# Kernel optimization log

Hardware: AMD Instinct MI355X
Metric: run time of the kernel (lower is better)

The kernel has to match this reference:

```python
import jax, jax.numpy as jnp
import numpy as np

DX = 1.0  # voxel_spacing

def _grad(t, axis):
    """Central difference along `axis` with replicate (Neumann) boundaries.
    Matches F.pad(mode='replicate') + conv3d with a +/-0.5 stencil."""
    pad = [(0, 0)] * t.ndim
    pad[axis] = (1, 1)
    p = jnp.pad(t, pad, mode='edge')
    n = p.shape[axis]
    fwd = jax.lax.slice_in_dim(p, 2, n, axis=axis)
    bwd = jax.lax.slice_in_dim(p, 0, n - 2, axis=axis)
    return (fwd - bwd) * (0.5 / DX)

# axis mapping for [B, C, D, H, W]: grad_x -> W (4), grad_y -> H (3), grad_z -> D (2)
_AXES = (4, 3, 2)

def setup_inputs() -> dict:
    key = jax.random.key(0)
    k1, k2, k3 = jax.random.split(key, 3)
    shape = (4, 1, 192, 192, 192)
    u = jax.random.uniform(k1, shape, dtype=jnp.float32)
    D = jax.random.uniform(k2, shape, dtype=jnp.float32)
    rho = jax.random.uniform(k3, shape, dtype=jnp.float32)
    return {"u": u, "D": D, "rho": rho}

def reference(u, D, rho):
    # div(D * grad(u))
    div = jnp.zeros_like(u)
    for ax in _AXES:
        flux = D * _grad(u, ax)
        div = div + _grad(flux, ax)
    # du/dt = div(D grad u) + rho * u * (1 - u)
    return div + rho * u * (1.0 - u)
```

## Files before the change

### kernel.cpp

```cpp
#include <hip/hip_runtime.h>


#define NX 192

__global__ __launch_bounds__(192)
void fk_kernel(const float* __restrict__ u,
               const float* __restrict__ Dd,
               const float* __restrict__ rho,
               float* __restrict__ out)
{
    const int x = threadIdx.x;
    int row = blockIdx.x;
    const int y = row % NX;
    row /= NX;
    const int z = row % NX;
    const int b = row / NX;

    const int base = ((b * NX + z) * NX + y) * NX + x;

    const float uc = u[base];

    auto divterm = [&](int c, int stride) -> float {
        const int n = NX;
        const int jp  = (c + 1 < n) ? (c + 1) : (n - 1);
        const int jm  = (c - 1 > 0) ? (c - 1) : 0;
        const int jpp = (jp + 1 < n) ? (jp + 1) : (n - 1);
        const int jpm = jp - 1;
        const int jmp = jm + 1;
        const int jmm = (jm - 1 > 0) ? (jm - 1) : 0;

        const float fp = Dd[base + (jp - c) * stride] *
                         (u[base + (jpp - c) * stride] - u[base + (jpm - c) * stride]);
        const float fm = Dd[base + (jm - c) * stride] *
                         (u[base + (jmp - c) * stride] - u[base + (jmm - c) * stride]);
        return (fp - fm) * 0.25f;
    };

    const float dx = divterm(x, 1);
    const float dy = divterm(y, NX);
    const float dz = divterm(z, NX * NX);

    const float reaction = rho[base] * uc * (1.0f - uc);

    out[base] = dx + dy + dz + reaction;
}

extern "C" void kernel_launch(void* const* d_in, const int* in_sizes, int n_in,
                              void* d_out, int out_size, void* d_ws, size_t ws_size,
                              hipStream_t stream) {
    const float* u   = (const float*)d_in[0];
    const float* Dd  = (const float*)d_in[1];
    const float* rho = (const float*)d_in[2];
    float* out = (float*)d_out;

    const int B = 4;
    const int rows = B * NX * NX;

    fk_kernel<<<rows, NX, 0, stream>>>(u, Dd, rho, out);
}
```

Measured before the change: 125.8 us.

## Vectorize stencil with float4 per thread and 4-row blocks

Each thread now computes four consecutive x outputs using float4 loads for u, D, rho and the y/z neighbor rows, with a fast interior path for the x stencil that reuses loaded values. Blocks become 48x4 threads covering four y rows, so neighboring rows share cache lines. This cuts the number of load instructions and redundant per-element neighbor loads in a memory-bound stencil. Boundary threads use a scalar fallback path, and fewer total threads may reduce latency hiding.

```diff
diff --git a/kernel.cpp b/kernel.cpp
--- a/kernel.cpp
+++ b/kernel.cpp
@@ -9,40 +9,98 @@
                const float* __restrict__ rho,
                float* __restrict__ out)
 {
-    const int x = threadIdx.x;
-    int row = blockIdx.x;
-    const int y = row % NX;
-    row /= NX;
-    const int z = row % NX;
-    const int b = row / NX;
+    const int tx = threadIdx.x;
+    const int ty = threadIdx.y;
+    int bid = blockIdx.x;
+    const int ytile = bid % 48;  bid /= 48;
+    const int z = bid % NX;
+    const int b = bid / NX;
+    const int y = ytile * 4 + ty;
+    const int x0 = tx * 4;
 
-    const int base = ((b * NX + z) * NX + y) * NX + x;
+    const int rowb = ((b * NX + z) * NX + y) * NX;
+    const int base = rowb + x0;
 
-    const float uc = u[base];
+    const float4 uc = *(const float4*)(u   + base);
+    const float4 dc = *(const float4*)(Dd  + base);
+    const float4 rc = *(const float4*)(rho + base);
 
-    auto divterm = [&](int c, int stride) -> float {
-        const int n = NX;
-        const int jp  = (c + 1 < n) ? (c + 1) : (n - 1);
-        const int jm  = (c - 1 > 0) ? (c - 1) : 0;
-        const int jpp = (jp + 1 < n) ? (jp + 1) : (n - 1);
+    float divx[4];
+    if (tx > 0 && tx < 47) {
+        const float um2 = u[base - 2], um1 = u[base - 1];
+        const float up1 = u[base + 4], up2 = u[base + 5];
+        const float dm1 = Dd[base - 1], dp1 = Dd[base + 4];
+        const float w[8] = {um2, um1, uc.x, uc.y, uc.z, uc.w, up1, up2};
+        const float d6[6] = {dm1, dc.x, dc.y, dc.z, dc.w, dp1};
+        #pragma unroll
+        for (int i = 0; i < 4; ++i) {
+            const float fp = d6[i + 2] * (w[i + 4] - w[i + 2]);
+            const float fm = d6[i]     * (w[i + 2] - w[i]);
+            divx[i] = (fp - fm) * 0.25f;
+        }
+    } else {
+        #pragma unroll
+        for (int i = 0; i < 4; ++i) {
+            const int c   = x0 + i;
+            const int jp  = (c + 1 < NX) ? (c + 1) : (NX - 1);
+            const int jm  = (c - 1 > 0) ? (c - 1) : 0;
+            const int jpp = (jp + 1 < NX) ? (jp + 1) : (NX - 1);
+            const int jpm = jp - 1;
+            const int jmp = jm + 1;
+            const int jmm = (jm - 1 > 0) ? (jm - 1) : 0;
+            const float fp = Dd[rowb + jp] * (u[rowb + jpp] - u[rowb + jpm]);
+            const float fm = Dd[rowb + jm] * (u[rowb + jmp] - u[rowb + jmm]);
+            divx[i] = (fp - fm) * 0.25f;
+        }
+    }
+
+    float4 divy4;
+    {
+        const int jp  = (y + 1 < NX) ? (y + 1) : (NX - 1);
+        const int jm  = (y - 1 > 0) ? (y - 1) : 0;
+        const int jpp = (jp + 1 < NX) ? (jp + 1) : (NX - 1);
         const int jpm = jp - 1;
         const int jmp = jm + 1;
         const int jmm = (jm - 1 > 0) ? (jm - 1) : 0;
+        const float4 upp = *(const float4*)(u  + base + (jpp - y) * NX);
+        const float4 upm = *(const float4*)(u  + base + (jpm - y) * NX);
+        const float4 ump = *(const float4*)(u  + base + (jmp - y) * NX);
+        const float4 umm = *(const float4*)(u  + base + (jmm - y) * NX);
+        const float4 djp = *(const float4*)(Dd + base + (jp  - y) * NX);
+        const float4 djm = *(const float4*)(Dd + base + (jm  - y) * NX);
+        divy4.x = (djp.x * (upp.x - upm.x) - djm.x * (ump.x - umm.x)) * 0.25f;
+        divy4.y = (djp.y * (upp.y - upm.y) - djm.y * (ump.y - umm.y)) * 0.25f;
+        divy4.z = (djp.z * (upp.z - upm.z) - djm.z * (ump.z - umm.z)) * 0.25f;
+        divy4.w = (djp.w * (upp.w - upm.w) - djm.w * (ump.w - umm.w)) * 0.25f;
+    }
 
-        const float fp = Dd[base + (jp - c) * stride] *
-                         (u[base + (jpp - c) * stride] - u[base + (jpm - c) * stride]);
-        const float fm = Dd[base + (jm - c) * stride] *
-                         (u[base + (jmp - c) * stride] - u[base + (jmm - c) * stride]);
-        return (fp - fm) * 0.25f;
-    };
+    float4 divz4;
+    {
+        const int S   = NX * NX;
+        const int jp  = (z + 1 < NX) ? (z + 1) : (NX - 1);
+        const int jm  = (z - 1 > 0) ? (z - 1) : 0;
+        const int jpp = (jp + 1 < NX) ? (jp + 1) : (NX - 1);
+        const int jpm = jp - 1;
+        const int jmp = jm + 1;
+        const int jmm = (jm - 1 > 0) ? (jm - 1) : 0;
+        const float4 upp = *(const float4*)(u  + base + (jpp - z) * S);
+        const float4 upm = *(const float4*)(u  + base + (jpm - z) * S);
+        const float4 ump = *(const float4*)(u  + base + (jmp - z) * S);
+        const float4 umm = *(const float4*)(u  + base + (jmm - z) * S);
+        const float4 djp = *(const float4*)(Dd + base + (jp  - z) * S);
+        const float4 djm = *(const float4*)(Dd + base + (jm  - z) * S);
+        divz4.x = (djp.x * (upp.x - upm.x) - djm.x * (ump.x - umm.x)) * 0.25f;
+        divz4.y = (djp.y * (upp.y - upm.y) - djm.y * (ump.y - umm.y)) * 0.25f;
+        divz4.z = (djp.z * (upp.z - upm.z) - djm.z * (ump.z - umm.z)) * 0.25f;
+        divz4.w = (djp.w * (upp.w - upm.w) - djm.w * (ump.w - umm.w)) * 0.25f;
+    }
 
-    const float dx = divterm(x, 1);
-    const float dy = divterm(y, NX);
-    const float dz = divterm(z, NX * NX);
-
-    const float reaction = rho[base] * uc * (1.0f - uc);
-
-    out[base] = dx + dy + dz + reaction;
+    float4 o;
+    o.x = divx[0] + divy4.x + divz4.x + rc.x * uc.x * (1.0f - uc.x);
+    o.y = divx[1] + divy4.y + divz4.y + rc.y * uc.y * (1.0f - uc.y);
+    o.z = divx[2] + divy4.z + divz4.z + rc.z * uc.z * (1.0f - uc.z);
+    o.w = divx[3] + divy4.w + divz4.w + rc.w * uc.w * (1.0f - uc.w);
+    *(float4*)(out + base) = o;
 }
 
 extern "C" void kernel_launch(void* const* d_in, const int* in_sizes, int n_in,
@@ -54,7 +112,7 @@
     float* out = (float*)d_out;
 
     const int B = 4;
-    const int rows = B * NX * NX;
-
-    fk_kernel<<<rows, NX, 0, stream>>>(u, Dd, rho, out);
+    dim3 block(48, 4, 1);
+    const int grid = B * NX * (NX / 4);
+    fk_kernel<<<grid, block, 0, stream>>>(u, Dd, rho, out);
 }
```

Result: slower. 143.7 us (+14.2%).

## Stream along z with register sliding window and float4 vectorized stencil

Applied to the files above, without the earlier changes.

Each thread now handles four x-points and marches through a chunk of 16 z-planes. The z-neighbours of u and D are kept in a rotating set of registers, so each plane is read once for the z-direction stencil instead of repeatedly. Loads and the output store use float4 vectors, and the x-halo comes from short neighbouring loads. The aim is to cut redundant global and cache traffic in this memory-bound stencil, at the cost of more registers, per-chunk z-halo reloads and extra boundary-handling branches.

```diff
diff --git a/kernel.cpp b/kernel.cpp
--- a/kernel.cpp
+++ b/kernel.cpp
@@ -1,48 +1,132 @@
 #include <hip/hip_runtime.h>
 
 
-#define NX 192
+#define NX  192
+#define SP  (NX * NX)
+#define ZCH 16
 
-__global__ __launch_bounds__(192)
+__global__ __launch_bounds__(192, 4)
 void fk_kernel(const float* __restrict__ u,
                const float* __restrict__ Dd,
                const float* __restrict__ rho,
                float* __restrict__ out)
 {
-    const int x = threadIdx.x;
-    int row = blockIdx.x;
-    const int y = row % NX;
-    row /= NX;
-    const int z = row % NX;
-    const int b = row / NX;
+    const int tx = threadIdx.x;
+    const int ty = threadIdx.y;
+    int bid = blockIdx.x;
+    const int ytile = bid % (NX / 4);   bid /= (NX / 4);
+    const int zc    = bid % (NX / ZCH); bid /= (NX / ZCH);
+    const int b     = bid;
+    const int y  = ytile * 4 + ty;
+    const int x0 = tx * 4;
+    const int z0 = zc * ZCH;
 
-    const int base = ((b * NX + z) * NX + y) * NX + x;
+    const int jpY  = (y + 1 < NX) ? y + 1 : NX - 1;
+    const int jmY  = (y - 1 > 0) ? y - 1 : 0;
+    const int jppY = (jpY + 1 < NX) ? jpY + 1 : NX - 1;
+    const int jpmY = jpY - 1;
+    const int jmpY = jmY + 1;
+    const int jmmY = (jmY - 1 > 0) ? jmY - 1 : 0;
+    const bool ld_jpm = (jpmY != y);
+    const bool ld_jmp = (jmpY != y);
+    const int o_jpp = (jppY - y) * NX;
+    const int o_jmm = (jmmY - y) * NX;
+    const int o_jpm = (jpmY - y) * NX;
+    const int o_jmp = (jmpY - y) * NX;
+    const int o_jp  = (jpY  - y) * NX;
+    const int o_jm  = (jmY  - y) * NX;
 
-    const float uc = u[base];
+    const int col0 = ((b * NX + z0) * NX + y) * NX + x0;
+    const float* pu = u   + col0;
+    const float* pd = Dd  + col0;
+    const float* pr = rho + col0;
+    float*       po = out + col0;
 
-    auto divterm = [&](int c, int stride) -> float {
-        const int n = NX;
-        const int jp  = (c + 1 < n) ? (c + 1) : (n - 1);
-        const int jm  = (c - 1 > 0) ? (c - 1) : 0;
-        const int jpp = (jp + 1 < n) ? (jp + 1) : (n - 1);
-        const int jpm = jp - 1;
-        const int jmp = jm + 1;
-        const int jmm = (jm - 1 > 0) ? (jm - 1) : 0;
+    const int zm1 = (z0 - 1 > 0) ? z0 - 1 : 0;
+    const int zm2 = (z0 - 2 > 0) ? z0 - 2 : 0;
+    float4 uz0 = *(const float4*)(pu + (zm2 - z0) * SP);
+    float4 uz1 = *(const float4*)(pu + (zm1 - z0) * SP);
+    float4 uz2 = *(const float4*)(pu);
+    float4 uz3 = *(const float4*)(pu + SP);
+    float4 uz4 = *(const float4*)(pu + 2 * SP);
+    float4 dz0 = *(const float4*)(pd + (zm1 - z0) * SP);
+    float4 dz1 = *(const float4*)(pd);
+    float4 dz2 = *(const float4*)(pd + SP);
 
-        const float fp = Dd[base + (jp - c) * stride] *
-                         (u[base + (jpp - c) * stride] - u[base + (jpm - c) * stride]);
-        const float fm = Dd[base + (jm - c) * stride] *
-                         (u[base + (jmp - c) * stride] - u[base + (jmm - c) * stride]);
-        return (fp - fm) * 0.25f;
-    };
+    #pragma unroll 4
+    for (int z = z0; z < z0 + ZCH; ++z) {
+        const int zp3 = (z + 3 < NX) ? z + 3 : NX - 1;
+        const int zp2 = (z + 2 < NX) ? z + 2 : NX - 1;
+        const float4 unx = *(const float4*)(pu + (zp3 - z) * SP);
+        const float4 dnx = *(const float4*)(pd + (zp2 - z) * SP);
+        const float4 rc  = *(const float4*)(pr);
 
-    const float dx = divterm(x, 1);
-    const float dy = divterm(y, NX);
-    const float dz = divterm(z, NX * NX);
+        const float4 u_jpp = *(const float4*)(pu + o_jpp);
+        const float4 u_jmm = *(const float4*)(pu + o_jmm);
+        const float4 d_jp  = *(const float4*)(pd + o_jp);
+        const float4 d_jm  = *(const float4*)(pd + o_jm);
+        float4 u_jpm = uz2, u_jmp = uz2;
+        if (ld_jpm) u_jpm = *(const float4*)(pu + o_jpm);
+        if (ld_jmp) u_jmp = *(const float4*)(pu + o_jmp);
 
-    const float reaction = rho[base] * uc * (1.0f - uc);
+        float um2, um1, up1, up2, dm1, dp1;
+        if (tx > 0) {
+            const float2 t = *(const float2*)(pu - 2);
+            um2 = t.x; um1 = t.y; dm1 = pd[-1];
+        } else { um2 = uz2.x; um1 = uz2.x; dm1 = dz1.x; }
+        if (tx < NX / 4 - 1) {
+            const float2 t = *(const float2*)(pu + 4);
+            up1 = t.x; up2 = t.y; dp1 = pd[4];
+        } else { up1 = uz2.w; up2 = uz2.w; dp1 = dz1.w; }
 
-    out[base] = dx + dy + dz + reaction;
+        const float w[8]  = {um2, um1, uz2.x, uz2.y, uz2.z, uz2.w, up1, up2};
+        const float d6[6] = {dm1, dz1.x, dz1.y, dz1.z, dz1.w, dp1};
+        float divx[4];
+        #pragma unroll
+        for (int i = 0; i < 4; ++i) {
+            const float fp = d6[i + 2] * (w[i + 4] - w[i + 2]);
+            const float fm = d6[i]     * (w[i + 2] - w[i]);
+            divx[i] = (fp - fm) * 0.25f;
+        }
+        if (tx == 0)
+            divx[0] = (d6[2] * (w[4] - w[2]) - dz1.x * (uz2.y - uz2.x)) * 0.25f;
+        if (tx == NX / 4 - 1)
+            divx[3] = (dz1.w * (uz2.w - uz2.z) - d6[3] * (w[5] - w[3])) * 0.25f;
+
+        float4 divy;
+        divy.x = (d_jp.x * (u_jpp.x - u_jpm.x) - d_jm.x * (u_jmp.x - u_jmm.x)) * 0.25f;
+        divy.y = (d_jp.y * (u_jpp.y - u_jpm.y) - d_jm.y * (u_jmp.y - u_jmm.y)) * 0.25f;
+        divy.z = (d_jp.z * (u_jpp.z - u_jpm.z) - d_jm.z * (u_jmp.z - u_jmm.z)) * 0.25f;
+        divy.w = (d_jp.w * (u_jpp.w - u_jpm.w) - d_jm.w * (u_jmp.w - u_jmm.w)) * 0.25f;
+
+        const bool zlo = (z == 0), zhi = (z == NX - 1);
+        float4 divz;
+        {
+            const float apx = zhi ? uz2.x : uz4.x, bpx = zhi ? uz1.x : uz2.x;
+            const float apy = zhi ? uz2.y : uz4.y, bpy = zhi ? uz1.y : uz2.y;
+            const float apz = zhi ? uz2.z : uz4.z, bpz = zhi ? uz1.z : uz2.z;
+            const float apw = zhi ? uz2.w : uz4.w, bpw = zhi ? uz1.w : uz2.w;
+            const float amx = zlo ? uz3.x : uz2.x, bmx = zlo ? uz2.x : uz0.x;
+            const float amy = zlo ? uz3.y : uz2.y, bmy = zlo ? uz2.y : uz0.y;
+            const float amz = zlo ? uz3.z : uz2.z, bmz = zlo ? uz2.z : uz0.z;
+            const float amw = zlo ? uz3.w : uz2.w, bmw = zlo ? uz2.w : uz0.w;
+            divz.x = (dz2.x * (apx - bpx) - dz0.x * (amx - bmx)) * 0.25f;
+            divz.y = (dz2.y * (apy - bpy) - dz0.y * (amy - bmy)) * 0.25f;
+            divz.z = (dz2.z * (apz - bpz) - dz0.z * (amz - bmz)) * 0.25f;
+            divz.w = (dz2.w * (apw - bpw) - dz0.w * (amw - bmw)) * 0.25f;
+        }
+
+        float4 o;
+        o.x = divx[0] + divy.x + divz.x + rc.x * uz2.x * (1.0f - uz2.x);
+        o.y = divx[1] + divy.y + divz.y + rc.y * uz2.y * (1.0f - uz2.y);
+        o.z = divx[2] + divy.z + divz.z + rc.z * uz2.z * (1.0f - uz2.z);
+        o.w = divx[3] + divy.w + divz.w + rc.w * uz2.w * (1.0f - uz2.w);
+        *(float4*)po = o;
+
+        uz0 = uz1; uz1 = uz2; uz2 = uz3; uz3 = uz4; uz4 = unx;
+        dz0 = dz1; dz1 = dz2; dz2 = dnx;
+        pu += SP; pd += SP; pr += SP; po += SP;
+    }
 }
 
 extern "C" void kernel_launch(void* const* d_in, const int* in_sizes, int n_in,
@@ -54,7 +138,7 @@
     float* out = (float*)d_out;
 
     const int B = 4;
-    const int rows = B * NX * NX;
-
-    fk_kernel<<<rows, NX, 0, stream>>>(u, Dd, rho, out);
+    dim3 block(NX / 4, 4, 1);
+    const int grid = B * (NX / ZCH) * (NX / 4);
+    fk_kernel<<<grid, block, 0, stream>>>(u, Dd, rho, out);
 }
```

Measured after the change: 134.5 us. 6.9% more time.

## Tile 3D stencil in shared memory with z-marching rolling slab buffers

Applied to the files above, without the earlier changes.

Replaces the one-thread-per-voxel kernel, which made many redundant global loads per output, with 64x16 xy tiles that march through 24-slice z chunks. A rolling five-slab u buffer and three-slab D buffer live in LDS, the next slice is prefetched into registers, and each thread computes two x-adjacent outputs with float2 LDS and global access. Global traffic drops to roughly one read per input element plus halos. The costs are large LDS use per block, which limits occupancy, two barriers per z step, and a grid of only 1152 blocks.

```diff
diff --git a/kernel.cpp b/kernel.cpp
--- a/kernel.cpp
+++ b/kernel.cpp
@@ -1,48 +1,168 @@
 #include <hip/hip_runtime.h>
 
 
-#define NX 192
+#define NX   192
+#define SP   (NX * NX)
+#define TX   64
+#define TY   16
+#define ZC   24
+#define LROW 68
+#define SLAB (20 * LROW)
 
-__global__ __launch_bounds__(192)
+#define LD2(p, o) (*(const float2*)((p) + (o)))
+
+__global__ __launch_bounds__(512, 4)
 void fk_kernel(const float* __restrict__ u,
                const float* __restrict__ Dd,
                const float* __restrict__ rho,
                float* __restrict__ out)
 {
-    const int x = threadIdx.x;
-    int row = blockIdx.x;
-    const int y = row % NX;
-    row /= NX;
-    const int z = row % NX;
-    const int b = row / NX;
+    __shared__ float Ush[5 * SLAB];
+    __shared__ float Dsh[3 * SLAB];
 
-    const int base = ((b * NX + z) * NX + y) * NX + x;
+    const int tx  = threadIdx.x;
+    const int ty  = threadIdx.y;
+    const int tid = ty * 32 + tx;
 
-    const float uc = u[base];
+    int bid = blockIdx.x;
+    const int xt = bid % 3;  bid /= 3;
+    const int yt = bid % 12; bid /= 12;
+    const int zc = bid % 8;  bid /= 8;
+    const int b  = bid;
 
-    auto divterm = [&](int c, int stride) -> float {
-        const int n = NX;
-        const int jp  = (c + 1 < n) ? (c + 1) : (n - 1);
-        const int jm  = (c - 1 > 0) ? (c - 1) : 0;
-        const int jpp = (jp + 1 < n) ? (jp + 1) : (n - 1);
-        const int jpm = jp - 1;
-        const int jmp = jm + 1;
-        const int jmm = (jm - 1 > 0) ? (jm - 1) : 0;
+    const int x0 = xt * TX, y0 = yt * TY, z0 = zc * ZC;
 
-        const float fp = Dd[base + (jp - c) * stride] *
-                         (u[base + (jpp - c) * stride] - u[base + (jpm - c) * stride]);
-        const float fm = Dd[base + (jm - c) * stride] *
-                         (u[base + (jmp - c) * stride] - u[base + (jmm - c) * stride]);
-        return (fp - fm) * 0.25f;
-    };
+    const size_t vol = (size_t)b * NX * SP;
+    const float* ub = u   + vol;
+    const float* db = Dd  + vol;
+    const float* rb = rho + vol;
+    float*       ob = out + vol;
 
-    const float dx = divterm(x, 1);
-    const float dy = divterm(y, NX);
-    const float dz = divterm(z, NX * NX);
+    int g0, g1, g2;
+    {
+        #pragma unroll
+        for (int k = 0; k < 3; ++k) {
+            const int p = tid + 512 * k;
+            const int pp = (p < SLAB) ? p : 0;
+            const int r = pp / LROW, c = pp % LROW;
+            int gy = y0 + r - 2; gy = gy < 0 ? 0 : (gy > NX - 1 ? NX - 1 : gy);
+            int gx = x0 + c - 2; gx = gx < 0 ? 0 : (gx > NX - 1 ? NX - 1 : gx);
+            const int go = gy * NX + gx;
+            if (k == 0) g0 = go; else if (k == 1) g1 = go; else g2 = go;
+        }
+    }
+    const bool a2 = (tid < SLAB - 1024);
 
-    const float reaction = rho[base] * uc * (1.0f - uc);
+    #pragma unroll
+    for (int s = 0; s < 5; ++s) {
+        int pz = z0 - 2 + s; pz = pz < 0 ? 0 : pz;
+        const float* src = ub + (size_t)pz * SP;
+        Ush[s * SLAB + tid]       = src[g0];
+        Ush[s * SLAB + tid + 512] = src[g1];
+        if (a2) Ush[s * SLAB + tid + 1024] = src[g2];
+    }
+    #pragma unroll
+    for (int s = 0; s < 3; ++s) {
+        int pz = z0 - 1 + s; pz = pz < 0 ? 0 : pz;
+        const float* src = db + (size_t)pz * SP;
+        Dsh[s * SLAB + tid]       = src[g0];
+        Dsh[s * SLAB + tid + 512] = src[g1];
+        if (a2) Dsh[s * SLAB + tid + 1024] = src[g2];
+    }
+    __syncthreads();
 
-    out[base] = dx + dy + dz + reaction;
+    int su0 = 0, su1 = 1, su2 = 2, su3 = 3, su4 = 4;
+    int sd0 = 0, sd1 = 1, sd2 = 2;
+
+    const int x  = x0 + 2 * tx;
+    const int y  = y0 + ty;
+    const int bl = (ty + 2) * LROW + (2 * tx + 2);
+    const size_t gcen = (size_t)y * NX + x;
+
+    const bool fx0 = (x == 0);
+    const bool fx1 = (x + 1 == NX - 1);
+    const bool fy0 = (y == 0);
+    const bool fy1 = (y == NX - 1);
+
+    for (int iz = 0; iz < ZC; ++iz) {
+        const int z = z0 + iz;
+        const bool pf = (iz + 1 < ZC);
+
+        float pu0, pu1, pu2, pd0, pd1, pd2;
+        if (pf) {
+            const int zu = (z + 3 > NX - 1) ? NX - 1 : z + 3;
+            const int zd = (z + 2 > NX - 1) ? NX - 1 : z + 2;
+            const float* us = ub + (size_t)zu * SP;
+            const float* ds = db + (size_t)zd * SP;
+            pu0 = us[g0]; pu1 = us[g1]; if (a2) pu2 = us[g2];
+            pd0 = ds[g0]; pd1 = ds[g1]; if (a2) pd2 = ds[g2];
+        }
+        const float2 rc = *(const float2*)(rb + (size_t)z * SP + gcen);
+
+        const float* Uc = Ush + su2 * SLAB;
+        const float* Dc = Dsh + sd1 * SLAB;
+        const float2 uc   = LD2(Uc, bl);
+        const float2 uxm  = LD2(Uc, bl - 2);
+        const float2 uxp  = LD2(Uc, bl + 2);
+        const float2 uym  = LD2(Uc, bl - 2 * LROW);
+        const float2 uyp  = LD2(Uc, bl + 2 * LROW);
+        const float2 dc   = LD2(Dc, bl);
+        const float2 dxm  = LD2(Dc, bl - 2);
+        const float2 dxp  = LD2(Dc, bl + 2);
+        const float2 dym  = LD2(Dc, bl - LROW);
+        const float2 dyp  = LD2(Dc, bl + LROW);
+        const float2 uzm2 = LD2(Ush + su0 * SLAB, bl);
+        const float2 uzp2 = LD2(Ush + su4 * SLAB, bl);
+        const float2 dzm  = LD2(Dsh + sd0 * SLAB, bl);
+        const float2 dzp  = LD2(Dsh + sd2 * SLAB, bl);
+
+        float divx_x = dc.y  * (uxp.x - uc.x) - dxm.y * (uc.x - uxm.x);
+        float divx_y = dxp.x * (uxp.y - uc.y) - dc.x  * (uc.y - uxm.y);
+        if (fx0) divx_x = dc.y * (uxp.x - uc.x) - dc.x * (uc.y - uc.x);
+        if (fx1) divx_y = dc.y * (uc.y - uc.x)  - dc.x * (uc.y - uxm.y);
+
+        float divy_x = dyp.x * (uyp.x - uc.x) - dym.x * (uc.x - uym.x);
+        float divy_y = dyp.y * (uyp.y - uc.y) - dym.y * (uc.y - uym.y);
+        if (fy0) {
+            const float2 uyp1 = LD2(Uc, bl + LROW);
+            divy_x = dyp.x * (uyp.x - uc.x) - dym.x * (uyp1.x - uc.x);
+            divy_y = dyp.y * (uyp.y - uc.y) - dym.y * (uyp1.y - uc.y);
+        }
+        if (fy1) {
+            const float2 uym1 = LD2(Uc, bl - LROW);
+            divy_x = dyp.x * (uc.x - uym1.x) - dym.x * (uc.x - uym.x);
+            divy_y = dyp.y * (uc.y - uym1.y) - dym.y * (uc.y - uym.y);
+        }
+
+        float divz_x = dzp.x * (uzp2.x - uc.x) - dzm.x * (uc.x - uzm2.x);
+        float divz_y = dzp.y * (uzp2.y - uc.y) - dzm.y * (uc.y - uzm2.y);
+        if (z == 0) {
+            const float2 uzp1 = LD2(Ush + su3 * SLAB, bl);
+            divz_x = dzp.x * (uzp2.x - uc.x) - dzm.x * (uzp1.x - uc.x);
+            divz_y = dzp.y * (uzp2.y - uc.y) - dzm.y * (uzp1.y - uc.y);
+        }
+        if (z == NX - 1) {
+            const float2 uzm1 = LD2(Ush + su1 * SLAB, bl);
+            divz_x = dzp.x * (uc.x - uzm1.x) - dzm.x * (uc.x - uzm2.x);
+            divz_y = dzp.y * (uc.y - uzm1.y) - dzm.y * (uc.y - uzm2.y);
+        }
+
+        float2 o;
+        o.x = 0.25f * (divx_x + divy_x + divz_x) + rc.x * uc.x * (1.0f - uc.x);
+        o.y = 0.25f * (divx_y + divy_y + divz_y) + rc.y * uc.y * (1.0f - uc.y);
+        *(float2*)(ob + (size_t)z * SP + gcen) = o;
+
+        __syncthreads();
+        if (pf) {
+            float* Uw = Ush + su0 * SLAB;
+            float* Dw = Dsh + sd0 * SLAB;
+            Uw[tid] = pu0; Uw[tid + 512] = pu1; if (a2) Uw[tid + 1024] = pu2;
+            Dw[tid] = pd0; Dw[tid + 512] = pd1; if (a2) Dw[tid + 1024] = pd2;
+            int t = su0; su0 = su1; su1 = su2; su2 = su3; su3 = su4; su4 = t;
+            t = sd0; sd0 = sd1; sd1 = sd2; sd2 = t;
+        }
+        __syncthreads();
+    }
 }
 
 extern "C" void kernel_launch(void* const* d_in, const int* in_sizes, int n_in,
@@ -53,8 +173,7 @@
     const float* rho = (const float*)d_in[2];
     float* out = (float*)d_out;
 
-    const int B = 4;
-    const int rows = B * NX * NX;
-
-    fk_kernel<<<rows, NX, 0, stream>>>(u, Dd, rho, out);
+    dim3 block(32, 16, 1);
+    const int grid = 3 * 12 * 8 * 4;
+    fk_kernel<<<grid, block, 0, stream>>>(u, Dd, rho, out);
 }
```

Result: faster. 110.8 us (-12.0%).
